# Kernel optimization log

Hardware: AMD Instinct MI355X
Metric: run time of the kernel (lower is better)

Reference implementation:

```python
import jax, jax.numpy as jnp
import numpy as np

NUM_LABELS = 64
START, END, PAD = 0, 1, 2
B, L, V, D = 128, 1024, 30000, 256


def make_transitions(key):
    # replicates CRF.init_weights
    t = jax.random.uniform(key, (NUM_LABELS, NUM_LABELS), minval=-0.1, maxval=0.1)
    t = t.at[:, START].set(-10000.0)
    t = t.at[END, :].set(-10000.0)
    t = t.at[PAD, :].set(-10000.0)
    t = t.at[:, PAD].set(-10000.0)
    t = t.at[PAD, PAD].set(0.0)
    t = t.at[PAD, END].set(0.0)
    return t.astype(jnp.float32)


def setup_inputs() -> dict:
    key = jax.random.key(0)
    k0, k1, k2, k3, k4 = jax.random.split(key, 5)
    x = jax.random.randint(k0, (B, L), 0, V)
    tags = jax.random.randint(k1, (B, L), 0, NUM_LABELS)
    mask = jnp.ones((B, L), dtype=jnp.float32)  # ignored by CRF (source passes mask=None)
    embed = jax.random.normal(k2, (V, D), dtype=jnp.float32)
    W = jax.random.normal(k3, (D, NUM_LABELS), dtype=jnp.float32) * 0.05
    b = jnp.zeros((NUM_LABELS,), dtype=jnp.float32)
    trans = make_transitions(k4)
    return {"x": x, "tags": tags, "mask": mask, "embed": embed, "W": W, "b": b, "trans": trans}


def _crf_nll(emissions, tags, trans):
    # emissions: [B, L, T]; tags: [B, L]; trans: [T, T]
    # NOTE: original CRF.forward ignores the user mask (passes mask=None ->
    # all-ones mask), so every position is valid and last tag is tags[:, -1].
    # gold path score
    e_scores = jnp.take_along_axis(emissions, tags[:, :, None], axis=2)[:, :, 0].sum(axis=1)
    t_scores = trans[tags[:, :-1], tags[:, 1:]].sum(axis=1)
    scores = e_scores + t_scores + trans[START, tags[:, 0]] + trans[tags[:, -1], END]
    # log partition: forward algorithm (log-space recursion over time)
    alpha0 = trans[START][None, :] + emissions[:, 0]  # [B, T]

    def step(alphas, emit_t):
        # alphas: [B, T_prev] -> logsumexp over previous tag
        new = jax.nn.logsumexp(alphas[:, :, None] + trans[None, :, :], axis=1) + emit_t
        return new, None

    alphas, _ = jax.lax.scan(step, alpha0, jnp.swapaxes(emissions[:, 1:], 0, 1))
    log_z = jax.nn.logsumexp(alphas + trans[:, END][None, :], axis=1)  # [B]
    return -jnp.sum(scores - log_z)


def reference(x, tags, mask, embed, W, b, trans):
    emissions = embed[x] @ W + b  # [B, L, T]
    return _crf_nll(emissions, tags, trans)
```

## Files before the change

### kernel.cpp

```cpp
#include <hip/hip_runtime.h>
#include <hip/hip_bf16.h>

#define B_ 128
#define L_ 1024
#define T_ 64

using short8 = __attribute__((ext_vector_type(8))) short;
using f32x4  = __attribute__((ext_vector_type(4))) float;
using f32x16 = __attribute__((ext_vector_type(16))) float;

static __device__ __forceinline__ unsigned short bfb(float x) {
  return __builtin_bit_cast(unsigned short, __float2bfloat16(x));
}
static __device__ __forceinline__ float asf(unsigned u) { return __builtin_bit_cast(float, u); }
static __device__ __forceinline__ float bf2f(unsigned short b) { return asf(((unsigned)b) << 16); }
static __device__ __forceinline__ unsigned pk2(float lo, float hi) {
  __hip_bfloat162 h = __float22bfloat162_rn(float2{lo, hi});
  unsigned u;
  __builtin_memcpy(&u, &h, 4);
  return u;
}
static __device__ __forceinline__ unsigned pk2t(float lo, float hi) {
  return __builtin_amdgcn_perm(__builtin_bit_cast(unsigned, hi),
                               __builtin_bit_cast(unsigned, lo), 0x07060302u);
}
static __device__ __forceinline__ void pswap(unsigned& x, unsigned& y) {
  asm("v_permlane32_swap_b32 %0, %1" : "+v"(x), "+v"(y));
}

__global__ __launch_bounds__(256) void k_prep(const float* __restrict__ trans,
                                              unsigned short* __restrict__ expET) {
  int t = blockIdx.x * 256 + threadIdx.x;
  expET[t] = bfb(__expf(trans[(t & 63) * T_ + (t >> 6)]));
}

__global__ __launch_bounds__(256) void k_emis(const int* __restrict__ x,
                                              const float* __restrict__ embed,
                                              const float* __restrict__ W,
                                              const float* __restrict__ bias,
                                              unsigned short* __restrict__ Fout) {
  const int L = threadIdx.x & 63, wv = threadIdx.x >> 6, m = L & 15, q = L >> 4;
  short8 Wf[8][4];
#pragma unroll
  for (int kap = 0; kap < 8; kap++)
#pragma unroll
    for (int u = 0; u < 4; u++) {
      short8 w;
#pragma unroll
      for (int d = 0; d < 8; d++)
        w[d] = (short)bfb(W[(32 * kap + 8 * q + d) * T_ + 16 * u + m]);
      Wf[kap][u] = w;
    }
  const float bj0 = bias[m], bj1 = bias[16 + m], bj2 = bias[32 + m], bj3 = bias[48 + m];
  for (int it = 0; it < 4; it++) {
    const int tokbase = ((blockIdx.x * 4 + wv) * 4 + it) * 16;
    const float* er = embed + (size_t)x[tokbase + m] * 256;
    f32x4 acc[4] = {{0.f,0.f,0.f,0.f},{0.f,0.f,0.f,0.f},{0.f,0.f,0.f,0.f},{0.f,0.f,0.f,0.f}};
#pragma unroll
    for (int kap = 0; kap < 8; kap++) {
      float4 p0 = *(const float4*)(er + 32 * kap + 8 * q);
      float4 p1 = *(const float4*)(er + 32 * kap + 8 * q + 4);
      unsigned u0 = pk2(p0.x, p0.y), u1 = pk2(p0.z, p0.w);
      unsigned u2 = pk2(p1.x, p1.y), u3 = pk2(p1.z, p1.w);
      short8 af = __builtin_bit_cast(short8, make_uint4(u0, u1, u2, u3));
#pragma unroll
      for (int u = 0; u < 4; u++)
        acc[u] = __builtin_amdgcn_mfma_f32_16x16x32_bf16(af, Wf[kap][u], acc[u], 0, 0, 0);
    }
#pragma unroll
    for (int r = 0; r < 4; r++) {
      float e0 = acc[0][r] + bj0, e1 = acc[1][r] + bj1;
      float e2 = acc[2][r] + bj2, e3 = acc[3][r] + bj3;
      float mr = fmaxf(fmaxf(e0, e1), fmaxf(e2, e3));
#pragma unroll
      for (int off = 1; off < 16; off <<= 1) mr = fmaxf(mr, __shfl_xor(mr, off));
      float x0 = __expf(e0 - mr), x1 = __expf(e1 - mr);
      float x2 = __expf(e2 - mr), x3 = __expf(e3 - mr);
      float sr = (x0 + x1) + (x2 + x3);
#pragma unroll
      for (int off = 1; off < 16; off <<= 1) sr += __shfl_xor(sr, off);
      float rs = 1.0f / sr;
      unsigned short* Fp = Fout + (size_t)(tokbase + 4 * q + r) * T_ + m;
      Fp[0]  = bfb(x0 * rs);
      Fp[16] = bfb(x1 * rs);
      Fp[32] = bfb(x2 * rs);
      Fp[48] = bfb(x3 * rs);
    }
  }
}

__global__ __launch_bounds__(64) void k_scan(const unsigned short* __restrict__ F,
                                             const unsigned short* __restrict__ expET,
                                             unsigned short* __restrict__ XT,
                                             float* __restrict__ rlog,
                                             int Cshift) {
  const int job = blockIdx.x;
  const int C = 1 << Cshift;
  const int c = job & (C - 1);
  const int b = job >> Cshift;
  const int K = (1023 + C - 1) >> Cshift;
  const int a = 1 + c * K;
  const int len = min(K, 1024 - a);
  const int L = threadIdx.x, nh = L & 31, hh = L >> 5;

  short8 Af[2][4];
#pragma unroll
  for (int I = 0; I < 2; I++)
#pragma unroll
    for (int kap = 0; kap < 4; kap++)
      Af[I][kap] = *(const short8*)(expET + (32 * I + nh) * T_ + 16 * kap + 8 * hh);

  unsigned Bf[4][2][4];
#pragma unroll
  for (int kap = 0; kap < 4; kap++)
#pragma unroll
    for (int J = 0; J < 2; J++)
#pragma unroll
      for (int dw = 0; dw < 4; dw++) {
        int k0 = 16 * kap + 8 * hh + 2 * dw, n = 32 * J + nh;
        unsigned u = 0;
        if (k0 == n) u = 0x3F80u;
        if (k0 + 1 == n) u = 0x3F800000u;
        Bf[kap][J][dw] = u;
      }

  const unsigned short* Fb = F + (size_t)b * (L_ * T_);
  uint2 Fc[2][4];
#pragma unroll
  for (int I = 0; I < 2; I++)
#pragma unroll
    for (int j = 0; j < 4; j++)
      Fc[I][j] = *(const uint2*)(Fb + (size_t)a * T_ + (16 * I + 4 * j + 2 * hh) * 2);

  float logacc = 0.f;
  unsigned PD[2][2][4][2];
  const f32x16 Z = {};

  for (int s = 0; s < len; s++) {
    f32x16 D[2][2];
#pragma unroll
    for (int I = 0; I < 2; I++)
#pragma unroll
      for (int J = 0; J < 2; J++) {
        short8 b0 = __builtin_bit_cast(short8,
            make_uint4(Bf[0][J][0], Bf[0][J][1], Bf[0][J][2], Bf[0][J][3]));
        f32x16 d = __builtin_amdgcn_mfma_f32_32x32x16_bf16(Af[I][0], b0, Z, 0, 0, 0);
#pragma unroll
        for (int kap = 1; kap < 4; kap++) {
          short8 bk = __builtin_bit_cast(short8,
              make_uint4(Bf[kap][J][0], Bf[kap][J][1], Bf[kap][J][2], Bf[kap][J][3]));
          d = __builtin_amdgcn_mfma_f32_32x32x16_bf16(Af[I][kap], bk, d, 0, 0, 0);
        }
        D[I][J] = d;
      }
    uint2 Fn[2][4];
    {
      const int ln = (s + 1 < len) ? (a + s + 1) : (a + s);
#pragma unroll
      for (int I = 0; I < 2; I++)
#pragma unroll
        for (int j = 0; j < 4; j++)
          Fn[I][j] = *(const uint2*)(Fb + (size_t)ln * T_ + (16 * I + 4 * j + 2 * hh) * 2);
    }
#pragma unroll
    for (int I = 0; I < 2; I++)
#pragma unroll
      for (int j = 0; j < 4; j++) {
        uint2 g = Fc[I][j];
        float f0 = asf(g.x << 16), f1 = asf(g.x & 0xffff0000u);
        float f2 = asf(g.y << 16), f3 = asf(g.y & 0xffff0000u);
#pragma unroll
        for (int J = 0; J < 2; J++) {
          D[I][J][4 * j + 0] *= f0;
          D[I][J][4 * j + 1] *= f1;
          D[I][J][4 * j + 2] *= f2;
          D[I][J][4 * j + 3] *= f3;
        }
      }
    if ((s & 15) == 15) {
      float mx = D[0][0][0];
#pragma unroll
      for (int I = 0; I < 2; I++)
#pragma unroll
        for (int J = 0; J < 2; J++)
#pragma unroll
        for (int r = 0; r < 16; r++) mx = fmaxf(mx, D[I][J][r]);
#pragma unroll
      for (int off = 1; off < 64; off <<= 1) mx = fmaxf(mx, __shfl_xor(mx, off));
      float rs = 1.0f / mx;
      logacc += __logf(mx);
#pragma unroll
      for (int I = 0; I < 2; I++)
#pragma unroll
        for (int J = 0; J < 2; J++)
#pragma unroll
        for (int r = 0; r < 16; r++) D[I][J][r] *= rs;
    }
#pragma unroll
    for (int I = 0; I < 2; I++)
#pragma unroll
      for (int J = 0; J < 2; J++)
#pragma unroll
        for (int j = 0; j < 4; j++) {
          PD[I][J][j][0] = pk2t(D[I][J][4 * j + 0], D[I][J][4 * j + 1]);
          PD[I][J][j][1] = pk2t(D[I][J][4 * j + 2], D[I][J][4 * j + 3]);
        }
#pragma unroll
    for (int I = 0; I < 2; I++)
#pragma unroll
      for (int j = 0; j < 4; j++) Fc[I][j] = Fn[I][j];
    if (s + 1 < len) {
#pragma unroll
      for (int kap = 0; kap < 4; kap++) {
        const int Ip = kap >> 1, e2 = 2 * (kap & 1);
#pragma unroll
        for (int J = 0; J < 2; J++) {
          unsigned x0 = PD[Ip][J][e2][0], y0 = PD[Ip][J][e2 + 1][0];
          unsigned x1 = PD[Ip][J][e2][1], y1 = PD[Ip][J][e2 + 1][1];
          pswap(x0, y0);
          pswap(x1, y1);
          Bf[kap][J][0] = x0;
          Bf[kap][J][1] = x1;
          Bf[kap][J][2] = y0;
          Bf[kap][J][3] = y1;
        }
      }
    }
  }
  unsigned* X2 = (unsigned*)(XT + (size_t)job * 4096);
#pragma unroll
  for (int I = 0; I < 2; I++)
#pragma unroll
    for (int J = 0; J < 2; J++)
#pragma unroll
      for (int j = 0; j < 4; j++) {
        X2[(32 * J + nh) * 32 + 16 * I + 4 * j + 2 * hh + 0] = PD[I][J][j][0];
        X2[(32 * J + nh) * 32 + 16 * I + 4 * j + 2 * hh + 1] = PD[I][J][j][1];
      }
  if (L == 0) rlog[job] = logacc;
}

__global__ __launch_bounds__(64) void k_apply(const unsigned short* __restrict__ XT,
                                              const float* __restrict__ rlog,
                                              const unsigned short* __restrict__ F,
                                              const float* __restrict__ trans,
                                              float* __restrict__ logz, int Cshift) {
  const int b = blockIdx.x, i = threadIdx.x;
  const int C = 1 << Cshift;
  __shared__ float vS[64];
  float v = __expf(trans[i]) * bf2f(F[(size_t)b * (L_ * T_) + i]);
  float lacc = 0.f;
  vS[i] = v;
  __syncthreads();
  for (int c = 0; c < C; c++) {
    const unsigned short* Xc = XT + (size_t)(b * C + c) * 4096;
    float a0 = 0.f, a1 = 0.f, a2 = 0.f, a3 = 0.f;
#pragma unroll
    for (int j = 0; j < 64; j += 4) {
      a0 = fmaf(bf2f(Xc[(j + 0) * T_ + i]), vS[j + 0], a0);
      a1 = fmaf(bf2f(Xc[(j + 1) * T_ + i]), vS[j + 1], a1);
      a2 = fmaf(bf2f(Xc[(j + 2) * T_ + i]), vS[j + 2], a2);
      a3 = fmaf(bf2f(Xc[(j + 3) * T_ + i]), vS[j + 3], a3);
    }
    float nv = (a0 + a1) + (a2 + a3);
    float mx = nv;
#pragma unroll
    for (int off = 1; off < 64; off <<= 1) mx = fmaxf(mx, __shfl_xor(mx, off));
    v = nv * (1.0f / mx);
    lacc += __logf(mx) + rlog[b * C + c];
    __syncthreads();
    vS[i] = v;
    __syncthreads();
  }
  float t = v * __expf(trans[i * T_ + 1]);
#pragma unroll
  for (int off = 1; off < 64; off <<= 1) t += __shfl_xor(t, off);
  if (i == 0) logz[b] = lacc + __logf(t);
}

__global__ __launch_bounds__(256) void k_scores(const int* __restrict__ tags,
                                                const unsigned short* __restrict__ F,
                                                const float* __restrict__ trans,
                                                float* __restrict__ score) {
  const int b = blockIdx.x;
  const int* tg = tags + (size_t)b * L_;
  const unsigned short* Fu = F + (size_t)b * (L_ * T_);
  float acc = 0.f;
  for (int l = threadIdx.x; l < L_; l += 256) {
    const int t = tg[l];
    acc += __logf(bf2f(Fu[(size_t)l * T_ + t]));
    if (l < L_ - 1) acc += trans[t * T_ + tg[l + 1]];
  }
#pragma unroll
  for (int off = 32; off > 0; off >>= 1) acc += __shfl_xor(acc, off);
  __shared__ float red[4];
  if ((threadIdx.x & 63) == 0) red[threadIdx.x >> 6] = acc;
  __syncthreads();
  if (threadIdx.x == 0) {
    float s = red[0] + red[1] + red[2] + red[3];
    s += trans[0 * T_ + tg[0]];
    s += trans[tg[L_ - 1] * T_ + 1];
    score[b] = s;
  }
}

__global__ __launch_bounds__(128) void k_final(const float* __restrict__ score,
                                               const float* __restrict__ logz,
                                               float* __restrict__ out) {
  const int t = threadIdx.x;
  float v = score[t] - logz[t];
#pragma unroll
  for (int off = 32; off > 0; off >>= 1) v += __shfl_xor(v, off);
  __shared__ float r[2];
  if ((t & 63) == 0) r[t >> 6] = v;
  __syncthreads();
  if (t == 0) out[0] = -(r[0] + r[1]);
}

extern "C" void kernel_launch(void* const* d_in, const int* in_sizes, int n_in,
                              void* d_out, int out_size, void* d_ws, size_t ws_size,
                              hipStream_t stream) {
  const int* x = (const int*)d_in[0];
  const int* tags = (const int*)d_in[1];
  const float* embed = (const float*)d_in[3];
  const float* W = (const float*)d_in[4];
  const float* bias = (const float*)d_in[5];
  const float* trans = (const float*)d_in[6];

  const size_t fbytes = (size_t)B_ * L_ * T_ * 2;
  int Cshift = 5;
  while (Cshift > 0) {
    size_t need = fbytes + (((size_t)1 << Cshift) * 1048576)
                  + (((size_t)128 << Cshift) * 4)
                  + 1024 + 8192;
    if (need <= ws_size) break;
    Cshift--;
  }
  const int C = 1 << Cshift;

  char* ws = (char*)d_ws;
  unsigned short* F = (unsigned short*)ws;
  unsigned short* XT = (unsigned short*)(ws + fbytes);
  float* rlog = (float*)(ws + fbytes + (size_t)C * 1048576);
  float* logz = (float*)((char*)rlog + (size_t)128 * C * 4);
  float* score = logz + B_;
  unsigned short* expET = (unsigned short*)((char*)logz + 1024);
  float* out = (float*)d_out;

  k_prep<<<16, 256, 0, stream>>>(trans, expET);
  k_emis<<<512, 256, 0, stream>>>(x, embed, W, bias, F);
  k_scan<<<128 * C, 64, 0, stream>>>(F, expET, XT, rlog, Cshift);
  k_apply<<<B_, 64, 0, stream>>>(XT, rlog, F, trans, logz, Cshift);
  k_scores<<<B_, 256, 0, stream>>>(tags, F, trans, score);
  k_final<<<1, 128, 0, stream>>>(score, logz, out);
}
```

Measured before the change: 233.7 us.

## Stage W via LDS, restructure chunk recurrence per-J, double chunk count

The emission kernel now converts W to bf16 once into a swizzled shared-memory buffer, and each lane loads its MFMA fragments with vector LDS reads instead of many strided global loads. The chunked forward-recurrence loop is reorganised to process one output column block J at a time, with the next-row prefetch issued before the MFMAs and the final-state store folded into the last iteration. This is meant to lower register pressure and overlap loads with compute. Cshift rises from 5 to 6, doubling the number of parallel time chunks per sequence when workspace allows, at the cost of more chunk-combine work in k_apply. The next-row prefetch is no longer clamped, so the last iteration reads one row past the chunk end.

```diff
diff --git a/kernel.cpp b/kernel.cpp
--- a/kernel.cpp
+++ b/kernel.cpp
@@ -39,18 +39,20 @@
                                               const float* __restrict__ W,
                                               const float* __restrict__ bias,
                                               unsigned short* __restrict__ Fout) {
+  __shared__ unsigned short Wsw[16384];
+  for (int e = threadIdx.x; e < 16384; e += 256) {
+    int k = e >> 6, n = e & 63;
+    int idx = ((k >> 5) << 11) + ((n >> 4) << 9) + (((k >> 3) & 3) << 7) + ((n & 15) << 3) + (k & 7);
+    Wsw[idx] = bfb(W[e]);
+  }
+  __syncthreads();
   const int L = threadIdx.x & 63, wv = threadIdx.x >> 6, m = L & 15, q = L >> 4;
   short8 Wf[8][4];
 #pragma unroll
-  for (int kap = 0; kap < 8; kap++)
-#pragma unroll
-    for (int u = 0; u < 4; u++) {
-      short8 w;
-#pragma unroll
-      for (int d = 0; d < 8; d++)
-        w[d] = (short)bfb(W[(32 * kap + 8 * q + d) * T_ + 16 * u + m]);
-      Wf[kap][u] = w;
-    }
+  for (int kk = 0; kk < 8; kk++)
+#pragma unroll
+    for (int u = 0; u < 4; u++)
+      Wf[kk][u] = *(const short8*)&Wsw[kk * 2048 + u * 512 + q * 128 + m * 8];
   const float bj0 = bias[m], bj1 = bias[16 + m], bj2 = bias[32 + m], bj3 = bias[48 + m];
   for (int it = 0; it < 4; it++) {
     const int tokbase = ((blockIdx.x * 4 + wv) * 4 + it) * 16;
@@ -133,15 +135,25 @@
       Fc[I][j] = *(const uint2*)(Fb + (size_t)a * T_ + (16 * I + 4 * j + 2 * hh) * 2);
 
   float logacc = 0.f;
-  unsigned PD[2][2][4][2];
   const f32x16 Z = {};
 
   for (int s = 0; s < len; s++) {
-    f32x16 D[2][2];
-#pragma unroll
-    for (int I = 0; I < 2; I++)
-#pragma unroll
-      for (int J = 0; J < 2; J++) {
+    uint2 Fn[2][4];
+    {
+      const unsigned short* Frow = Fb + (size_t)(a + s + 1) * T_;
+#pragma unroll
+      for (int I = 0; I < 2; I++)
+#pragma unroll
+        for (int j = 0; j < 4; j++)
+          Fn[I][j] = *(const uint2*)(Frow + (16 * I + 4 * j + 2 * hh) * 2);
+    }
+    const bool rn = ((s & 15) == 15);
+    float rs = 1.0f;
+#pragma unroll
+    for (int J = 0; J < 2; J++) {
+      f32x16 D[2];
+#pragma unroll
+      for (int I = 0; I < 2; I++) {
         short8 b0 = __builtin_bit_cast(short8,
             make_uint4(Bf[0][J][0], Bf[0][J][1], Bf[0][J][2], Bf[0][J][3]));
         f32x16 d = __builtin_amdgcn_mfma_f32_32x32x16_bf16(Af[I][0], b0, Z, 0, 0, 0);
@@ -151,72 +163,60 @@
               make_uint4(Bf[kap][J][0], Bf[kap][J][1], Bf[kap][J][2], Bf[kap][J][3]));
           d = __builtin_amdgcn_mfma_f32_32x32x16_bf16(Af[I][kap], bk, d, 0, 0, 0);
         }
-        D[I][J] = d;
+        D[I] = d;
       }
-    uint2 Fn[2][4];
-    {
-      const int ln = (s + 1 < len) ? (a + s + 1) : (a + s);
 #pragma unroll
       for (int I = 0; I < 2; I++)
 #pragma unroll
-        for (int j = 0; j < 4; j++)
-          Fn[I][j] = *(const uint2*)(Fb + (size_t)ln * T_ + (16 * I + 4 * j + 2 * hh) * 2);
-    }
-#pragma unroll
-    for (int I = 0; I < 2; I++)
-#pragma unroll
-      for (int j = 0; j < 4; j++) {
-        uint2 g = Fc[I][j];
-        float f0 = asf(g.x << 16), f1 = asf(g.x & 0xffff0000u);
-        float f2 = asf(g.y << 16), f3 = asf(g.y & 0xffff0000u);
-#pragma unroll
-        for (int J = 0; J < 2; J++) {
-          D[I][J][4 * j + 0] *= f0;
-          D[I][J][4 * j + 1] *= f1;
-          D[I][J][4 * j + 2] *= f2;
-          D[I][J][4 * j + 3] *= f3;
-        }
+        for (int j = 0; j < 4; j++) {
+          uint2 g = Fc[I][j];
+          float f0 = asf(g.x << 16), f1 = asf(g.x & 0xffff0000u);
+          float f2 = asf(g.y << 16), f3 = asf(g.y & 0xffff0000u);
+          D[I][4 * j + 0] *= f0;
+          D[I][4 * j + 1] *= f1;
+          D[I][4 * j + 2] *= f2;
+          D[I][4 * j + 3] *= f3;
+        }
+      if (rn) {
+        if (J == 0) {
+          float mx = D[0][0];
+#pragma unroll
+          for (int I = 0; I < 2; I++)
+#pragma unroll
+            for (int r = 0; r < 16; r++) mx = fmaxf(mx, D[I][r]);
+#pragma unroll
+          for (int off = 1; off < 64; off <<= 1) mx = fmaxf(mx, __shfl_xor(mx, off));
+          rs = 1.0f / mx;
+          logacc += __logf(mx);
+        }
+#pragma unroll
+        for (int I = 0; I < 2; I++)
+#pragma unroll
+          for (int r = 0; r < 16; r++) D[I][r] *= rs;
       }
-    if ((s & 15) == 15) {
-      float mx = D[0][0][0];
+      unsigned PDt[2][4][2];
 #pragma unroll
       for (int I = 0; I < 2; I++)
 #pragma unroll
-        for (int J = 0; J < 2; J++)
-#pragma unroll
-        for (int r = 0; r < 16; r++) mx = fmaxf(mx, D[I][J][r]);
-#pragma unroll
-      for (int off = 1; off < 64; off <<= 1) mx = fmaxf(mx, __shfl_xor(mx, off));
-      float rs = 1.0f / mx;
-      logacc += __logf(mx);
-#pragma unroll
-      for (int I = 0; I < 2; I++)
-#pragma unroll
-        for (int J = 0; J < 2; J++)
-#pragma unroll
-        for (int r = 0; r < 16; r++) D[I][J][r] *= rs;
-    }
-#pragma unroll
-    for (int I = 0; I < 2; I++)
-#pragma unroll
-      for (int J = 0; J < 2; J++)
-#pragma unroll
         for (int j = 0; j < 4; j++) {
-          PD[I][J][j][0] = pk2t(D[I][J][4 * j + 0], D[I][J][4 * j + 1]);
-          PD[I][J][j][1] = pk2t(D[I][J][4 * j + 2], D[I][J][4 * j + 3]);
-        }
-#pragma unroll
-    for (int I = 0; I < 2; I++)
-#pragma unroll
-      for (int j = 0; j < 4; j++) Fc[I][j] = Fn[I][j];
-    if (s + 1 < len) {
-#pragma unroll
-      for (int kap = 0; kap < 4; kap++) {
-        const int Ip = kap >> 1, e2 = 2 * (kap & 1);
-#pragma unroll
-        for (int J = 0; J < 2; J++) {
-          unsigned x0 = PD[Ip][J][e2][0], y0 = PD[Ip][J][e2 + 1][0];
-          unsigned x1 = PD[Ip][J][e2][1], y1 = PD[Ip][J][e2 + 1][1];
+          PDt[I][j][0] = pk2t(D[I][4 * j + 0], D[I][4 * j + 1]);
+          PDt[I][j][1] = pk2t(D[I][4 * j + 2], D[I][4 * j + 3]);
+        }
+      if (s == len - 1) {
+        unsigned* X2 = (unsigned*)(XT + (size_t)job * 4096) + (32 * J + nh) * 32;
+#pragma unroll
+        for (int I = 0; I < 2; I++)
+#pragma unroll
+          for (int j = 0; j < 4; j++) {
+            X2[16 * I + 4 * j + 2 * hh + 0] = PDt[I][j][0];
+            X2[16 * I + 4 * j + 2 * hh + 1] = PDt[I][j][1];
+          }
+      } else {
+#pragma unroll
+        for (int kap = 0; kap < 4; kap++) {
+          const int Ip = kap >> 1, e2 = 2 * (kap & 1);
+          unsigned x0 = PDt[Ip][e2][0], y0 = PDt[Ip][e2 + 1][0];
+          unsigned x1 = PDt[Ip][e2][1], y1 = PDt[Ip][e2 + 1][1];
           pswap(x0, y0);
           pswap(x1, y1);
           Bf[kap][J][0] = x0;
@@ -226,17 +226,11 @@
         }
       }
     }
-  }
-  unsigned* X2 = (unsigned*)(XT + (size_t)job * 4096);
-#pragma unroll
-  for (int I = 0; I < 2; I++)
-#pragma unroll
-    for (int J = 0; J < 2; J++)
-#pragma unroll
-      for (int j = 0; j < 4; j++) {
-        X2[(32 * J + nh) * 32 + 16 * I + 4 * j + 2 * hh + 0] = PD[I][J][j][0];
-        X2[(32 * J + nh) * 32 + 16 * I + 4 * j + 2 * hh + 1] = PD[I][J][j][1];
-      }
+#pragma unroll
+    for (int I = 0; I < 2; I++)
+#pragma unroll
+      for (int j = 0; j < 4; j++) Fc[I][j] = Fn[I][j];
+  }
   if (L == 0) rlog[job] = logacc;
 }
 
@@ -328,7 +322,7 @@
   const float* trans = (const float*)d_in[6];
 
   const size_t fbytes = (size_t)B_ * L_ * T_ * 2;
-  int Cshift = 5;
+  int Cshift = 6;
   while (Cshift > 0) {
     size_t need = fbytes + (((size_t)1 << Cshift) * 1048576)
                   + (((size_t)128 << Cshift) * 4)
```

New measurement: 267.5 us. 14.5% more time.
